# Performance work log

Measured on AMD Instinct MI355X. Metric: run time of the kernel, lower is better.

Reference implementation:

```python
import jax, jax.numpy as jnp
import numpy as np

B, N, DEG = 128, 512, 8          # graphs, nodes per graph, avg degree
E = B * N * DEG                  # 524288 edges
F_IN, H1, H2, C = 128, 64, 128, 10
RATIO = 0.8
K = int(np.ceil(RATIO * N))      # TopKPooling keeps ceil(0.8*N)=410 nodes per graph


def setup_inputs() -> dict:
    key = jax.random.key(0)
    ks = jax.random.split(key, 10)
    n_nodes = B * N
    x = jax.random.normal(ks[0], (n_nodes, F_IN), dtype=jnp.float32)
    # random intra-graph edges, then offset node ids per graph
    src = jax.random.randint(ks[1], (B, N * DEG), 0, N)
    dst = jax.random.randint(ks[2], (B, N * DEG), 0, N)
    off = (jnp.arange(B) * N)[:, None]
    edge_index = jnp.stack([(src + off).reshape(-1), (dst + off).reshape(-1)]).astype(jnp.int64)
    batch = jnp.repeat(jnp.arange(B), N).astype(jnp.int64)
    s1 = 1.0 / np.sqrt(F_IN)
    s2 = 1.0 / np.sqrt(H1)
    s3 = 1.0 / np.sqrt(H2)
    return {
        "x": x,
        "edge_index": edge_index,
        "batch": batch,
        "W1": jax.random.uniform(ks[3], (F_IN, H1), jnp.float32, -s1, s1),
        "b1": jnp.zeros((H1,), jnp.float32),
        "W2": jax.random.uniform(ks[4], (H1, H2), jnp.float32, -s2, s2),
        "b2": jnp.zeros((H2,), jnp.float32),
        "pool_w": jax.random.uniform(ks[5], (H2,), jnp.float32, -s3, s3),
        "fc_W": jax.random.uniform(ks[6], (H2, C), jnp.float32, -s3, s3),
        "fc_b": jax.random.uniform(ks[7], (C,), jnp.float32, -s3, s3),
    }


def gcn_conv(x, W, b, src, dst, num_nodes):
    # PyG GCNConv: add self-loops, symmetric normalization, scatter-add aggregation
    loop = jnp.arange(num_nodes)
    src = jnp.concatenate([src, loop])
    dst = jnp.concatenate([dst, loop])
    deg = jax.ops.segment_sum(jnp.ones_like(src, dtype=x.dtype), dst, num_segments=num_nodes)
    dis = jnp.where(deg > 0, jax.lax.rsqrt(jnp.maximum(deg, 1.0)), 0.0)
    norm = dis[src] * dis[dst]                       # [E+N]
    h = x @ W                                        # transform first (smaller of the two in conv1)
    out = jax.ops.segment_sum(norm[:, None] * h[src], dst, num_segments=num_nodes)
    return out + b


def reference(x, edge_index, batch, W1, b1, W2, b2, pool_w, fc_W, fc_b):
    num_nodes = x.shape[0]
    src, dst = edge_index[0], edge_index[1]
    x = jax.nn.relu(gcn_conv(x, W1, b1, src, dst, num_nodes))
    x = jax.nn.relu(gcn_conv(x, W2, b2, src, dst, num_nodes))
    # TopKPooling: score = (x . w)/||w||, per-graph top-k on raw score, gate by tanh(score)
    score = (x @ pool_w) / jnp.linalg.norm(pool_w)   # [B*N]
    score_b = score.reshape(B, N)
    top_vals, top_idx = jax.lax.top_k(score_b, K)    # [B, K]
    x_b = x.reshape(B, N, H2)
    x_sel = jnp.take_along_axis(x_b, top_idx[:, :, None], axis=1)   # [B, K, H2]
    x_sel = x_sel * jnp.tanh(top_vals)[:, :, None]
    # global max pool over each (pooled) graph; pooled edge_index is unused downstream
    g = jnp.max(x_sel, axis=1)                        # [B, H2]
    logits = g @ fc_W + fc_b                          # [B, C]
    return jax.nn.log_softmax(logits, axis=1)
```

## Files before the change

kernel.cpp:

```cpp
#include <hip/hip_runtime.h>
#include <hip/hip_bf16.h>


#define BB 128
#define NN 512
#define NODES (BB*NN)
#define EE (BB*NN*8)
#define EDGPG (NN*8)
#define F_IN 128
#define H1 64
#define H2 128
#define NC 10
#define KSEL 410
#define ROWCAP 48

typedef unsigned short u16;
typedef unsigned int   u32;

static __device__ __forceinline__ float lo2f(u32 u){ return __uint_as_float(u << 16); }
static __device__ __forceinline__ float hi2f(u32 u){ return __uint_as_float(u & 0xffff0000u); }
static __device__ __forceinline__ u16 f2b(float f){
    __hip_bfloat16 h = __float2bfloat16(f);
    return *reinterpret_cast<u16*>(&h);
}
static __device__ __forceinline__ u32 packbf(float a, float b){
    return (u32)f2b(a) | ((u32)f2b(b) << 16);
}
static __device__ __forceinline__ void acc8s(float* a, uint4 v, float ds){
    a[0] = fmaf(ds, lo2f(v.x), a[0]); a[1] = fmaf(ds, hi2f(v.x), a[1]);
    a[2] = fmaf(ds, lo2f(v.y), a[2]); a[3] = fmaf(ds, hi2f(v.y), a[3]);
    a[4] = fmaf(ds, lo2f(v.z), a[4]); a[5] = fmaf(ds, hi2f(v.z), a[5]);
    a[6] = fmaf(ds, lo2f(v.w), a[6]); a[7] = fmaf(ds, hi2f(v.w), a[7]);
}
static __device__ __forceinline__ void acc8(float* a, uint4 v){
    a[0] += lo2f(v.x); a[1] += hi2f(v.x);
    a[2] += lo2f(v.y); a[3] += hi2f(v.y);
    a[4] += lo2f(v.z); a[5] += hi2f(v.z);
    a[6] += lo2f(v.w); a[7] += hi2f(v.w);
}
static __device__ __forceinline__ int swz2048(int bid){
    return ((bid & 7) << 8) | (bid >> 3);
}

static __device__ __forceinline__ bool ei_is_i64(const int* __restrict__ ei){
    return ((ei[1] | ei[3] | ei[5] | ei[7]) == 0);
}
static __device__ __forceinline__ int ld_src(const int* __restrict__ ei, int e, bool w64){
    return w64 ? ei[2*e] : ei[e];
}
static __device__ __forceinline__ int ld_dst(const int* __restrict__ ei, int e, bool w64){
    return w64 ? ei[2*(EE + e)] : ei[EE + e];
}

#define G1NODES 64
#define XPAD 68
__global__ __launch_bounds__(512) void k_prep_gemm1(const int* __restrict__ ei,
                                                    const float* __restrict__ x,
                                                    const float* __restrict__ W1,
                                                    int* __restrict__ cnt,
                                                    int* __restrict__ adj,
                                                    u32* __restrict__ h1u){
    __shared__ __align__(16) float Ws[64*H1];
    __shared__ __align__(16) float xs[G1NODES*XPAD];
    bool w64 = ei_is_i64(ei);
    int t = threadIdx.x;
    int gb = (int)blockIdx.x;
    int b  = gb >> 3;
    int sub = gb & 7;
    int node0 = b*NN + sub*G1NODES;

    {
        int e = b*EDGPG + sub*512 + t;
        int d = (ld_dst(ei, e, w64) - b*NN) & (NN - 1);
        int s = ld_src(ei, e, w64) & (NODES - 1);
        int node = b*NN + d;
        int p = atomicAdd(&cnt[node], 1);
        if (p < ROWCAP - 1) adj[node*ROWCAP + 1 + p] = s;
    }
    if (t < G1NODES){
        int node = node0 + t;
        adj[node*ROWCAP] = node;
    }

    int tc = t & 15, tr = t >> 4;
    int j0 = tc*4, n0 = tr*2;
    float acc[2][4] = {};
    for (int half = 0; half < 2; ++half){
        const float4* Wv = (const float4*)(W1 + half*4096);
        for (int i = t; i < 1024; i += 512)
            *(float4*)&Ws[i*4] = Wv[i];
        for (int i = t; i < 1024; i += 512){
            int node = i >> 4, c = i & 15;
            float4 v = *(const float4*)(x + (size_t)(node0 + node)*F_IN + half*64 + c*4);
            *(float4*)&xs[node*XPAD + c*4] = v;
        }
        __syncthreads();
        #pragma unroll 2
        for (int k = 0; k < 64; k += 4){
            float4 xv0 = *(const float4*)&xs[(n0+0)*XPAD + k];
            float4 xv1 = *(const float4*)&xs[(n0+1)*XPAD + k];
            float xa0[4] = {xv0.x, xv0.y, xv0.z, xv0.w};
            float xa1[4] = {xv1.x, xv1.y, xv1.z, xv1.w};
            #pragma unroll
            for (int kk = 0; kk < 4; ++kk){
                float4 wv = *(const float4*)&Ws[(k+kk)*H1 + j0];
                acc[0][0] += xa0[kk]*wv.x; acc[0][1] += xa0[kk]*wv.y; acc[0][2] += xa0[kk]*wv.z; acc[0][3] += xa0[kk]*wv.w;
                acc[1][0] += xa1[kk]*wv.x; acc[1][1] += xa1[kk]*wv.y; acc[1][2] += xa1[kk]*wv.z; acc[1][3] += xa1[kk]*wv.w;
            }
        }
        __syncthreads();
    }
    #pragma unroll
    for (int i = 0; i < 2; ++i){
        int node = node0 + n0 + i;
        size_t base = (size_t)node*32 + tc*2;
        h1u[base]     = packbf(acc[i][0], acc[i][1]);
        h1u[base + 1] = packbf(acc[i][2], acc[i][3]);
    }
}

__global__ __launch_bounds__(256) void k_agg1(const uint4* __restrict__ h1v,
                                              const int* __restrict__ cnt,
                                              const int* __restrict__ adj,
                                              const float4* __restrict__ b1v,
                                              uint4* __restrict__ a1v){
    __shared__ float disl[NN];
    int t = threadIdx.x;
    int lb = swz2048((int)blockIdx.x);
    int node0 = lb*32;
    int gbase = node0 & ~(NN - 1);
    for (int i = t; i < NN; i += 256){
        int c = cnt[gbase + i]; if (c > ROWCAP-1) c = ROWCAP-1;
        disl[i] = rsqrtf((float)(c + 1));
    }
    __syncthreads();
    int node = node0 + (t >> 3);
    int fl = t & 7;
    int rs = node*ROWCAP;
    int c = cnt[node]; if (c > ROWCAP-1) c = ROWCAP-1;
    int pe = rs + c + 1;
    float a0[8] = {}, a1r[8] = {}, a2r[8] = {}, a3r[8] = {};
    int p = rs;
    for (; p + 4 <= pe; p += 4){
        int s0 = adj[p], s1 = adj[p+1], s2 = adj[p+2], s3 = adj[p+3];
        float d0 = disl[s0 & (NN-1)], d1 = disl[s1 & (NN-1)];
        float d2 = disl[s2 & (NN-1)], d3 = disl[s3 & (NN-1)];
        uint4 v0 = h1v[s0*8 + fl];
        uint4 v1 = h1v[s1*8 + fl];
        uint4 v2 = h1v[s2*8 + fl];
        uint4 v3 = h1v[s3*8 + fl];
        acc8s(a0, v0, d0); acc8s(a1r, v1, d1); acc8s(a2r, v2, d2); acc8s(a3r, v3, d3);
    }
    for (; p < pe; ++p){
        int s = adj[p];
        acc8s(a0, h1v[s*8 + fl], disl[s & (NN-1)]);
    }
    float r[8];
    #pragma unroll
    for (int j = 0; j < 8; ++j) r[j] = (a0[j] + a1r[j]) + (a2r[j] + a3r[j]);
    float dn = disl[node & (NN-1)];
    float4 bA = b1v[2*fl], bB = b1v[2*fl+1];
    float w0 = dn*r[0] + bA.x; w0 = w0 > 0.f ? w0 : 0.f;
    float w1 = dn*r[1] + bA.y; w1 = w1 > 0.f ? w1 : 0.f;
    float w2 = dn*r[2] + bA.z; w2 = w2 > 0.f ? w2 : 0.f;
    float w3 = dn*r[3] + bA.w; w3 = w3 > 0.f ? w3 : 0.f;
    float w4 = dn*r[4] + bB.x; w4 = w4 > 0.f ? w4 : 0.f;
    float w5 = dn*r[5] + bB.y; w5 = w5 > 0.f ? w5 : 0.f;
    float w6 = dn*r[6] + bB.z; w6 = w6 > 0.f ? w6 : 0.f;
    float w7 = dn*r[7] + bB.w; w7 = w7 > 0.f ? w7 : 0.f;
    a1v[node*8 + fl] = make_uint4(packbf(dn*w0, dn*w1), packbf(dn*w2, dn*w3),
                                  packbf(dn*w4, dn*w5), packbf(dn*w6, dn*w7));
}

#define G2NODES 32
#define APAD 68
__global__ __launch_bounds__(256) void k_gemm2s(const uint4* __restrict__ a1v,
                                                const int* __restrict__ cnt,
                                                const int* __restrict__ adj,
                                                const float* __restrict__ W2,
                                                const float* __restrict__ b2,
                                                const float* __restrict__ pw,
                                                u32* __restrict__ a2u,
                                                float* __restrict__ score){
    __shared__ __align__(16) float Ws[32*H2];
    __shared__ __align__(16) float as[G2NODES*APAD];
    __shared__ float pws[H2];
    int t = threadIdx.x;
    int lb = swz2048((int)blockIdx.x);
    int node0 = lb*G2NODES;
    if (t < H2) pws[t] = pw[t];
    {
        int fl = t & 7, nl = t >> 3;
        int node = node0 + nl;
        int rs = node*ROWCAP;
        int c = cnt[node]; if (c > ROWCAP-1) c = ROWCAP-1;
        int pe = rs + c + 1;
        float a0[8] = {}, a1r[8] = {}, a2r[8] = {}, a3r[8] = {};
        int p = rs;
        for (; p + 4 <= pe; p += 4){
            int s0 = adj[p], s1 = adj[p+1], s2 = adj[p+2], s3 = adj[p+3];
            uint4 v0 = a1v[s0*8 + fl];
            uint4 v1 = a1v[s1*8 + fl];
            uint4 v2 = a1v[s2*8 + fl];
            uint4 v3 = a1v[s3*8 + fl];
            acc8(a0, v0); acc8(a1r, v1); acc8(a2r, v2); acc8(a3r, v3);
        }
        for (; p < pe; ++p){
            uint4 v = a1v[adj[p]*8 + fl];
            acc8(a0, v);
        }
        float dn = rsqrtf((float)(c + 1));
        float* dst = &as[nl*APAD + 8*fl];
        float r0 = dn*((a0[0] + a1r[0]) + (a2r[0] + a3r[0]));
        float r1 = dn*((a0[1] + a1r[1]) + (a2r[1] + a3r[1]));
        float r2 = dn*((a0[2] + a1r[2]) + (a2r[2] + a3r[2]));
        float r3 = dn*((a0[3] + a1r[3]) + (a2r[3] + a3r[3]));
        float r4 = dn*((a0[4] + a1r[4]) + (a2r[4] + a3r[4]));
        float r5 = dn*((a0[5] + a1r[5]) + (a2r[5] + a3r[5]));
        float r6 = dn*((a0[6] + a1r[6]) + (a2r[6] + a3r[6]));
        float r7 = dn*((a0[7] + a1r[7]) + (a2r[7] + a3r[7]));
        *(float4*)&dst[0] = make_float4(r0, r1, r2, r3);
        *(float4*)&dst[4] = make_float4(r4, r5, r6, r7);
    }
    int tc = t & 31, tr = t >> 5;
    int j0 = tc*4, n0 = tr*4;
    float acc[4][4] = {};
    for (int half = 0; half < 2; ++half){
        const float4* Wv = (const float4*)(W2 + half*4096);
        for (int i = t; i < 1024; i += 256)
            *(float4*)&Ws[i*4] = Wv[i];
        __syncthreads();
        int kb = half*32;
        #pragma unroll 2
        for (int k = 0; k < 32; k += 4){
            float4 xv0 = *(const float4*)&as[(n0+0)*APAD + kb + k];
            float4 xv1 = *(const float4*)&as[(n0+1)*APAD + kb + k];
            float4 xv2 = *(const float4*)&as[(n0+2)*APAD + kb + k];
            float4 xv3 = *(const float4*)&as[(n0+3)*APAD + kb + k];
            float xa0[4] = {xv0.x, xv0.y, xv0.z, xv0.w};
            float xa1[4] = {xv1.x, xv1.y, xv1.z, xv1.w};
            float xa2[4] = {xv2.x, xv2.y, xv2.z, xv2.w};
            float xa3[4] = {xv3.x, xv3.y, xv3.z, xv3.w};
            #pragma unroll
            for (int kk = 0; kk < 4; ++kk){
                float4 wv = *(const float4*)&Ws[(k+kk)*H2 + j0];
                acc[0][0] += xa0[kk]*wv.x; acc[0][1] += xa0[kk]*wv.y; acc[0][2] += xa0[kk]*wv.z; acc[0][3] += xa0[kk]*wv.w;
                acc[1][0] += xa1[kk]*wv.x; acc[1][1] += xa1[kk]*wv.y; acc[1][2] += xa1[kk]*wv.z; acc[1][3] += xa1[kk]*wv.w;
                acc[2][0] += xa2[kk]*wv.x; acc[2][1] += xa2[kk]*wv.y; acc[2][2] += xa2[kk]*wv.z; acc[2][3] += xa2[kk]*wv.w;
                acc[3][0] += xa3[kk]*wv.x; acc[3][1] += xa3[kk]*wv.y; acc[3][2] += xa3[kk]*wv.z; acc[3][3] += xa3[kk]*wv.w;
            }
        }
        __syncthreads();
    }
    float p0 = pws[j0], p1 = pws[j0+1], p2 = pws[j0+2], p3 = pws[j0+3];
    float bj0 = b2[j0], bj1 = b2[j0+1], bj2 = b2[j0+2], bj3 = b2[j0+3];
    #pragma unroll
    for (int i = 0; i < 4; ++i){
        float v0 = acc[i][0] + bj0; v0 = v0 > 0.f ? v0 : 0.f;
        float v1 = acc[i][1] + bj1; v1 = v1 > 0.f ? v1 : 0.f;
        float v2 = acc[i][2] + bj2; v2 = v2 > 0.f ? v2 : 0.f;
        float v3 = acc[i][3] + bj3; v3 = v3 > 0.f ? v3 : 0.f;
        size_t base = (size_t)(node0 + n0 + i)*64 + tc*2;
        a2u[base]     = packbf(v0, v1);
        a2u[base + 1] = packbf(v2, v3);
        float sp = v0*p0 + v1*p1 + v2*p2 + v3*p3;
        sp += __shfl_xor(sp, 16, 32);
        sp += __shfl_xor(sp,  8, 32);
        sp += __shfl_xor(sp,  4, 32);
        sp += __shfl_xor(sp,  2, 32);
        sp += __shfl_xor(sp,  1, 32);
        if (tc == 0) score[node0 + n0 + i] = sp;
    }
}

__global__ __launch_bounds__(512) void k_pool(const u32* __restrict__ a2u,
                                              const float* __restrict__ score,
                                              const float* __restrict__ pw,
                                              const float* __restrict__ fcW,
                                              const float* __restrict__ fcb,
                                              float* __restrict__ out){
    __shared__ float so[NN];
    __shared__ float ss[NN];
    __shared__ float th[NN];
    __shared__ float pm[32*H2];
    __shared__ float gl[H2];
    __shared__ float fws[H2*NC];
    __shared__ float lg[NC];
    __shared__ float red[3];
    int b = blockIdx.x, t = threadIdx.x;
    for (int i = t; i < H2*NC; i += 512) fws[i] = fcW[i];
    if (t < H2){ float v = pw[t]; gl[t] = v*v; }
    __syncthreads();
    if (t == 0){
        float s = 0.f;
        for (int i = 0; i < H2; ++i) s += gl[i];
        red[2] = rsqrtf(s);
    }
    __syncthreads();
    float pwinv = red[2];
    float sc = score[b*NN + t];
    so[t] = sc; ss[t] = sc; th[t] = tanhf(sc*pwinv);
    __syncthreads();
    for (int k = 2; k <= NN; k <<= 1){
        for (int j = k >> 1; j > 0; j >>= 1){
            int ixj = t ^ j;
            if (ixj > t){
                float a = ss[t], c = ss[ixj];
                bool desc = ((t & k) == 0);
                bool sw = desc ? (a < c) : (a > c);
                if (sw){ ss[t] = c; ss[ixj] = a; }
            }
            __syncthreads();
        }
    }
    float thresh = ss[KSEL-1];
    float mask_t = (so[t] >= thresh) ? 0.f : -INFINITY;
    __syncthreads();
    so[t] = mask_t;
    __syncthreads();
    int tc = t & 15, q = t >> 4;
    const uint4* ap = (const uint4*)(a2u + (size_t)b*NN*64);
    float m0 = -INFINITY, m1 = -INFINITY, m2 = -INFINITY, m3 = -INFINITY;
    float m4 = -INFINITY, m5 = -INFINITY, m6 = -INFINITY, m7 = -INFINITY;
    int nb = q*16;
    #pragma unroll 4
    for (int n = nb; n < nb + 16; ++n){
        uint4 v = ap[(size_t)n*16 + tc];
        float thn = th[n], son = so[n];
        m0 = fmaxf(m0, lo2f(v.x)*thn + son);
        m1 = fmaxf(m1, hi2f(v.x)*thn + son);
        m2 = fmaxf(m2, lo2f(v.y)*thn + son);
        m3 = fmaxf(m3, hi2f(v.y)*thn + son);
        m4 = fmaxf(m4, lo2f(v.z)*thn + son);
        m5 = fmaxf(m5, hi2f(v.z)*thn + son);
        m6 = fmaxf(m6, lo2f(v.w)*thn + son);
        m7 = fmaxf(m7, hi2f(v.w)*thn + son);
    }
    float* pmr = &pm[q*H2 + 8*tc];
    pmr[0] = m0; pmr[1] = m1; pmr[2] = m2; pmr[3] = m3;
    pmr[4] = m4; pmr[5] = m5; pmr[6] = m6; pmr[7] = m7;
    __syncthreads();
    if (t < H2){
        float g = pm[t];
        #pragma unroll
        for (int qq = 1; qq < 32; ++qq) g = fmaxf(g, pm[qq*H2 + t]);
        gl[t] = g;
    }
    __syncthreads();
    if (t < NC){
        float acc = fcb[t];
        for (int k2 = 0; k2 < H2; ++k2) acc += gl[k2]*fws[k2*NC + t];
        lg[t] = acc;
    }
    __syncthreads();
    if (t == 0){
        float mx = lg[0];
        for (int i = 1; i < NC; ++i) mx = fmaxf(mx, lg[i]);
        float s = 0.f;
        for (int i = 0; i < NC; ++i) s += expf(lg[i] - mx);
        red[0] = mx; red[1] = logf(s);
    }
    __syncthreads();
    if (t < NC) out[b*NC + t] = lg[t] - red[0] - red[1];
}

extern "C" void kernel_launch(void* const* d_in, const int* in_sizes, int n_in,
                              void* d_out, int out_size, void* d_ws, size_t ws_size,
                              hipStream_t stream) {
    const float* x   = (const float*)d_in[0];
    const int*   ei  = (const int*)d_in[1];
    const float* W1  = (const float*)d_in[3];
    const float* b1  = (const float*)d_in[4];
    const float* W2  = (const float*)d_in[5];
    const float* b2  = (const float*)d_in[6];
    const float* pw  = (const float*)d_in[7];
    const float* fcW = (const float*)d_in[8];
    const float* fcb = (const float*)d_in[9];

    char* ws = (char*)d_ws;
    int*   cnt   = (int*)(ws + 4096);
    float* score = (float*)(ws + 524288);
    int*   adj   = (int*)(ws + 4194304);
    u32*   h1u   = (u32*)(ws + 16777216);
    u32*   a1u   = (u32*)(ws + 25165824);
    u32*   a2u   = (u32*)(ws + 33554432);

    hipMemsetAsync(cnt, 0, NODES*sizeof(int), stream);
    k_prep_gemm1<<<NODES/G1NODES, 512, 0, stream>>>(ei, x, W1, cnt, adj, h1u);
    k_agg1<<<NODES/32, 256, 0, stream>>>((const uint4*)h1u, cnt, adj,
                                         (const float4*)b1, (uint4*)a1u);
    k_gemm2s<<<NODES/G2NODES, 256, 0, stream>>>((const uint4*)a1u, cnt, adj,
                                                W2, b2, pw, a2u, score);
    k_pool<<<BB, 512, 0, stream>>>(a2u, score, pw, fcW, fcb, (float*)d_out);
}
```

Measured before the change: 173.8 us.

## Fuse GCN pipeline into two per-graph kernels with LDS-resident features

Replaces the four-kernel pipeline with two kernels that each run one 1024-thread block per graph. The first builds the adjacency (as u16 local ids) with LDS atomics, runs the W1 GEMM into a shared bf16 buffer, and aggregates conv1 from LDS. The second keeps a1, W2, scores and activations in LDS and fuses conv2 aggregation, the GEMM, scoring, top-k selection, gated max-pool and the FC/log-softmax. The goal is to remove the memset, the global h1, a2 and score round-trips and three kernel launch boundaries. In exchange, only 128 blocks run, which leaves many CUs idle. LDS use per block is close to the hardware limit, so each block runs long and serialized.

```diff
diff --git a/kernel.cpp b/kernel.cpp
--- a/kernel.cpp
+++ b/kernel.cpp
@@ -4,7 +4,6 @@
 
 #define BB 128
 #define NN 512
-#define NODES (BB*NN)
 #define EE (BB*NN*8)
 #define EDGPG (NN*8)
 #define F_IN 128
@@ -26,20 +25,25 @@
 static __device__ __forceinline__ u32 packbf(float a, float b){
     return (u32)f2b(a) | ((u32)f2b(b) << 16);
 }
-static __device__ __forceinline__ void acc8s(float* a, uint4 v, float ds){
-    a[0] = fmaf(ds, lo2f(v.x), a[0]); a[1] = fmaf(ds, hi2f(v.x), a[1]);
-    a[2] = fmaf(ds, lo2f(v.y), a[2]); a[3] = fmaf(ds, hi2f(v.y), a[3]);
-    a[4] = fmaf(ds, lo2f(v.z), a[4]); a[5] = fmaf(ds, hi2f(v.z), a[5]);
-    a[6] = fmaf(ds, lo2f(v.w), a[6]); a[7] = fmaf(ds, hi2f(v.w), a[7]);
-}
 static __device__ __forceinline__ void acc8(float* a, uint4 v){
     a[0] += lo2f(v.x); a[1] += hi2f(v.x);
     a[2] += lo2f(v.y); a[3] += hi2f(v.y);
     a[4] += lo2f(v.z); a[5] += hi2f(v.z);
     a[6] += lo2f(v.w); a[7] += hi2f(v.w);
 }
-static __device__ __forceinline__ int swz2048(int bid){
-    return ((bid & 7) << 8) | (bid >> 3);
+static __device__ __forceinline__ void acc32s(float* a, const u32* hrow, float ds){
+    #pragma unroll
+    for (int q = 0; q < 4; ++q){
+        uint4 v = *(const uint4*)(hrow + q*4);
+        a[q*8+0] = fmaf(ds, lo2f(v.x), a[q*8+0]);
+        a[q*8+1] = fmaf(ds, hi2f(v.x), a[q*8+1]);
+        a[q*8+2] = fmaf(ds, lo2f(v.y), a[q*8+2]);
+        a[q*8+3] = fmaf(ds, hi2f(v.y), a[q*8+3]);
+        a[q*8+4] = fmaf(ds, lo2f(v.z), a[q*8+4]);
+        a[q*8+5] = fmaf(ds, hi2f(v.z), a[q*8+5]);
+        a[q*8+6] = fmaf(ds, lo2f(v.w), a[q*8+6]);
+        a[q*8+7] = fmaf(ds, hi2f(v.w), a[q*8+7]);
+    }
 }
 
 static __device__ __forceinline__ bool ei_is_i64(const int* __restrict__ ei){
@@ -52,305 +56,315 @@
     return w64 ? ei[2*(EE + e)] : ei[EE + e];
 }
 
-#define G1NODES 64
-#define XPAD 68
-__global__ __launch_bounds__(512) void k_prep_gemm1(const int* __restrict__ ei,
-                                                    const float* __restrict__ x,
-                                                    const float* __restrict__ W1,
-                                                    int* __restrict__ cnt,
-                                                    int* __restrict__ adj,
-                                                    u32* __restrict__ h1u){
-    __shared__ __align__(16) float Ws[64*H1];
-    __shared__ __align__(16) float xs[G1NODES*XPAD];
+#define XP2 132
+#define H1R 36
+
+__global__ __launch_bounds__(1024) void k_conv1(const int* __restrict__ ei,
+                                                const float* __restrict__ x,
+                                                const float* __restrict__ W1,
+                                                const float* __restrict__ b1,
+                                                u16* __restrict__ adjG,
+                                                int* __restrict__ cntG,
+                                                uint4* __restrict__ a1u){
+    __shared__ int   cntL[NN];
+    __shared__ float disl[NN];
+    __shared__ float b1s[H1];
+    __shared__ __align__(16) float Ws[F_IN*H1];
+    __shared__ __align__(16) float xs[64*XP2];
+    __shared__ __align__(16) u32   h1g[NN*H1R];
     bool w64 = ei_is_i64(ei);
     int t = threadIdx.x;
-    int gb = (int)blockIdx.x;
-    int b  = gb >> 3;
-    int sub = gb & 7;
-    int node0 = b*NN + sub*G1NODES;
-
+    int g = blockIdx.x;
+
+    if (t < NN) cntL[t] = 0;
+    if (t < H1) b1s[t] = b1[t];
     {
-        int e = b*EDGPG + sub*512 + t;
-        int d = (ld_dst(ei, e, w64) - b*NN) & (NN - 1);
-        int s = ld_src(ei, e, w64) & (NODES - 1);
-        int node = b*NN + d;
-        int p = atomicAdd(&cnt[node], 1);
-        if (p < ROWCAP - 1) adj[node*ROWCAP + 1 + p] = s;
-    }
-    if (t < G1NODES){
-        int node = node0 + t;
-        adj[node*ROWCAP] = node;
-    }
+        const float4* Wv = (const float4*)W1;
+        *(float4*)&Ws[t*4]          = Wv[t];
+        *(float4*)&Ws[(t+1024)*4]   = Wv[t+1024];
+    }
+    __syncthreads();
+
+    #pragma unroll
+    for (int i = 0; i < 4; ++i){
+        int e = g*EDGPG + i*1024 + t;
+        int d = (ld_dst(ei, e, w64) - g*NN) & (NN - 1);
+        int s =  ld_src(ei, e, w64) & (NN - 1);
+        int p = atomicAdd(&cntL[d], 1);
+        if (p < ROWCAP - 1) adjG[(size_t)(g*NN + d)*ROWCAP + 1 + p] = (u16)s;
+    }
+    if (t < NN) adjG[(size_t)(g*NN + t)*ROWCAP] = (u16)t;
 
     int tc = t & 15, tr = t >> 4;
-    int j0 = tc*4, n0 = tr*2;
-    float acc[2][4] = {};
-    for (int half = 0; half < 2; ++half){
-        const float4* Wv = (const float4*)(W1 + half*4096);
-        for (int i = t; i < 1024; i += 512)
-            *(float4*)&Ws[i*4] = Wv[i];
-        for (int i = t; i < 1024; i += 512){
-            int node = i >> 4, c = i & 15;
-            float4 v = *(const float4*)(x + (size_t)(node0 + node)*F_IN + half*64 + c*4);
-            *(float4*)&xs[node*XPAD + c*4] = v;
+    int j0 = tc*4;
+    for (int c = 0; c < 8; ++c){
+        #pragma unroll
+        for (int kf = 0; kf < 2; ++kf){
+            int idx = t + kf*1024;
+            int row = idx >> 5, cf = idx & 31;
+            float4 v = *(const float4*)(x + (size_t)(g*NN + c*64 + row)*F_IN + cf*4);
+            *(float4*)&xs[row*XP2 + cf*4] = v;
         }
         __syncthreads();
-        #pragma unroll 2
-        for (int k = 0; k < 64; k += 4){
-            float4 xv0 = *(const float4*)&xs[(n0+0)*XPAD + k];
-            float4 xv1 = *(const float4*)&xs[(n0+1)*XPAD + k];
+        float a0 = 0.f, a1_ = 0.f, a2_ = 0.f, a3_ = 0.f;
+        #pragma unroll 4
+        for (int k = 0; k < F_IN; k += 4){
+            float4 xv = *(const float4*)&xs[tr*XP2 + k];
+            float xa[4] = {xv.x, xv.y, xv.z, xv.w};
+            #pragma unroll
+            for (int kk = 0; kk < 4; ++kk){
+                float4 wv = *(const float4*)&Ws[(k+kk)*H1 + j0];
+                a0 += xa[kk]*wv.x; a1_ += xa[kk]*wv.y;
+                a2_ += xa[kk]*wv.z; a3_ += xa[kk]*wv.w;
+            }
+        }
+        u32* hp = &h1g[(c*64 + tr)*H1R + tc*2];
+        hp[0] = packbf(a0, a1_);
+        hp[1] = packbf(a2_, a3_);
+        __syncthreads();
+    }
+
+    if (t < NN){
+        int c2 = cntL[t]; if (c2 > ROWCAP-1) c2 = ROWCAP-1;
+        cntG[g*NN + t] = c2;
+        disl[t] = rsqrtf((float)(c2 + 1));
+    }
+    __syncthreads();
+
+    {
+        int node = t >> 1, fl = t & 1;
+        int pe = cntL[node]; if (pe > ROWCAP-1) pe = ROWCAP-1;
+        pe += 1;
+        const u16* row = adjG + (size_t)(g*NN + node)*ROWCAP;
+        float acc[32] = {};
+        int p = 0;
+        for (; p + 4 <= pe; p += 4){
+            int s0 = row[p], s1 = row[p+1], s2 = row[p+2], s3 = row[p+3];
+            acc32s(acc, &h1g[s0*H1R + fl*16], disl[s0]);
+            acc32s(acc, &h1g[s1*H1R + fl*16], disl[s1]);
+            acc32s(acc, &h1g[s2*H1R + fl*16], disl[s2]);
+            acc32s(acc, &h1g[s3*H1R + fl*16], disl[s3]);
+        }
+        for (; p < pe; ++p){
+            int s = row[p];
+            acc32s(acc, &h1g[s*H1R + fl*16], disl[s]);
+        }
+        float dn = disl[node];
+        #pragma unroll
+        for (int q = 0; q < 4; ++q){
+            float v0 = fmaf(dn, acc[8*q+0], b1s[fl*32+8*q+0]); v0 = v0 > 0.f ? v0 : 0.f;
+            float v1 = fmaf(dn, acc[8*q+1], b1s[fl*32+8*q+1]); v1 = v1 > 0.f ? v1 : 0.f;
+            float v2 = fmaf(dn, acc[8*q+2], b1s[fl*32+8*q+2]); v2 = v2 > 0.f ? v2 : 0.f;
+            float v3 = fmaf(dn, acc[8*q+3], b1s[fl*32+8*q+3]); v3 = v3 > 0.f ? v3 : 0.f;
+            float v4 = fmaf(dn, acc[8*q+4], b1s[fl*32+8*q+4]); v4 = v4 > 0.f ? v4 : 0.f;
+            float v5 = fmaf(dn, acc[8*q+5], b1s[fl*32+8*q+5]); v5 = v5 > 0.f ? v5 : 0.f;
+            float v6 = fmaf(dn, acc[8*q+6], b1s[fl*32+8*q+6]); v6 = v6 > 0.f ? v6 : 0.f;
+            float v7 = fmaf(dn, acc[8*q+7], b1s[fl*32+8*q+7]); v7 = v7 > 0.f ? v7 : 0.f;
+            a1u[(size_t)(g*NN + node)*8 + fl*4 + q] =
+                make_uint4(packbf(dn*v0, dn*v1), packbf(dn*v2, dn*v3),
+                           packbf(dn*v4, dn*v5), packbf(dn*v6, dn*v7));
+        }
+    }
+}
+
+#define A1R 9
+#define AP2 68
+
+__global__ __launch_bounds__(1024) void k_conv2pool(const uint4* __restrict__ a1u,
+                                                    const u16* __restrict__ adjG,
+                                                    const int* __restrict__ cntG,
+                                                    const float* __restrict__ W2,
+                                                    const float* __restrict__ b2,
+                                                    const float* __restrict__ pw,
+                                                    const float* __restrict__ fcW,
+                                                    const float* __restrict__ fcb,
+                                                    float* __restrict__ out){
+    __shared__ __align__(16) uint4 a1g[NN*A1R];
+    __shared__ __align__(16) float W2pm[64*H2];
+    __shared__ __align__(16) float ass[128*AP2];
+    __shared__ float pws[H2], b2s[H2], gl[H2];
+    __shared__ int   cnti[NN];
+    __shared__ float disl[NN];
+    __shared__ float score_s[NN], th[NN], so[NN], ssort[NN];
+    __shared__ float fws[H2*NC];
+    __shared__ float lg[NC];
+    __shared__ float red[4];
+    int t = threadIdx.x;
+    int g = blockIdx.x;
+
+    #pragma unroll
+    for (int kf = 0; kf < 4; ++kf){
+        int idx = t + kf*1024;
+        a1g[(idx >> 3)*A1R + (idx & 7)] = a1u[(size_t)g*NN*8 + idx];
+    }
+    {
+        const float4* Wv = (const float4*)W2;
+        *(float4*)&W2pm[t*4]        = Wv[t];
+        *(float4*)&W2pm[(t+1024)*4] = Wv[t+1024];
+    }
+    if (t < H2){ pws[t] = pw[t]; b2s[t] = b2[t]; }
+    if (t < NN){
+        int c = cntG[g*NN + t];
+        cnti[t] = c;
+        disl[t] = rsqrtf((float)(c + 1));
+    }
+    for (int i = t; i < H2*NC; i += 1024) fws[i] = fcW[i];
+    __syncthreads();
+
+    int tc = t & 15, tr = t >> 4;
+    int j0 = tc*8;
+    u32 a2r[4][2][4];
+
+    #pragma unroll
+    for (int c = 0; c < 4; ++c){
+        {
+            int fl = t & 7, nl = t >> 3;
+            int node = c*128 + nl;
+            int pe = cnti[node] + 1;
+            const u16* row = adjG + (size_t)(g*NN + node)*ROWCAP;
+            float a0[8] = {}, b0[8] = {}, c0[8] = {}, d0[8] = {};
+            int p = 0;
+            for (; p + 4 <= pe; p += 4){
+                int s0 = row[p], s1 = row[p+1], s2 = row[p+2], s3 = row[p+3];
+                uint4 v0 = a1g[s0*A1R + fl];
+                uint4 v1 = a1g[s1*A1R + fl];
+                uint4 v2 = a1g[s2*A1R + fl];
+                uint4 v3 = a1g[s3*A1R + fl];
+                acc8(a0, v0); acc8(b0, v1); acc8(c0, v2); acc8(d0, v3);
+            }
+            for (; p < pe; ++p) acc8(a0, a1g[row[p]*A1R + fl]);
+            float dn = disl[node];
+            float* dst = &ass[nl*AP2 + fl*8];
+            float r0 = dn*((a0[0]+b0[0]) + (c0[0]+d0[0]));
+            float r1 = dn*((a0[1]+b0[1]) + (c0[1]+d0[1]));
+            float r2 = dn*((a0[2]+b0[2]) + (c0[2]+d0[2]));
+            float r3 = dn*((a0[3]+b0[3]) + (c0[3]+d0[3]));
+            float r4 = dn*((a0[4]+b0[4]) + (c0[4]+d0[4]));
+            float r5 = dn*((a0[5]+b0[5]) + (c0[5]+d0[5]));
+            float r6 = dn*((a0[6]+b0[6]) + (c0[6]+d0[6]));
+            float r7 = dn*((a0[7]+b0[7]) + (c0[7]+d0[7]));
+            *(float4*)&dst[0] = make_float4(r0, r1, r2, r3);
+            *(float4*)&dst[4] = make_float4(r4, r5, r6, r7);
+        }
+        __syncthreads();
+        float acc[2][8] = {};
+        #pragma unroll 4
+        for (int k = 0; k < H1; k += 4){
+            float4 xv0 = *(const float4*)&ass[(tr     )*AP2 + k];
+            float4 xv1 = *(const float4*)&ass[(tr + 64)*AP2 + k];
             float xa0[4] = {xv0.x, xv0.y, xv0.z, xv0.w};
             float xa1[4] = {xv1.x, xv1.y, xv1.z, xv1.w};
             #pragma unroll
             for (int kk = 0; kk < 4; ++kk){
-                float4 wv = *(const float4*)&Ws[(k+kk)*H1 + j0];
-                acc[0][0] += xa0[kk]*wv.x; acc[0][1] += xa0[kk]*wv.y; acc[0][2] += xa0[kk]*wv.z; acc[0][3] += xa0[kk]*wv.w;
-                acc[1][0] += xa1[kk]*wv.x; acc[1][1] += xa1[kk]*wv.y; acc[1][2] += xa1[kk]*wv.z; acc[1][3] += xa1[kk]*wv.w;
-            }
+                float4 wa = *(const float4*)&W2pm[(k+kk)*H2 + j0];
+                float4 wb = *(const float4*)&W2pm[(k+kk)*H2 + j0 + 4];
+                acc[0][0] += xa0[kk]*wa.x; acc[0][1] += xa0[kk]*wa.y;
+                acc[0][2] += xa0[kk]*wa.z; acc[0][3] += xa0[kk]*wa.w;
+                acc[0][4] += xa0[kk]*wb.x; acc[0][5] += xa0[kk]*wb.y;
+                acc[0][6] += xa0[kk]*wb.z; acc[0][7] += xa0[kk]*wb.w;
+                acc[1][0] += xa1[kk]*wa.x; acc[1][1] += xa1[kk]*wa.y;
+                acc[1][2] += xa1[kk]*wa.z; acc[1][3] += xa1[kk]*wa.w;
+                acc[1][4] += xa1[kk]*wb.x; acc[1][5] += xa1[kk]*wb.y;
+                acc[1][6] += xa1[kk]*wb.z; acc[1][7] += xa1[kk]*wb.w;
+            }
+        }
+        #pragma unroll
+        for (int r2 = 0; r2 < 2; ++r2){
+            float v0 = acc[r2][0] + b2s[j0+0]; v0 = v0 > 0.f ? v0 : 0.f;
+            float v1 = acc[r2][1] + b2s[j0+1]; v1 = v1 > 0.f ? v1 : 0.f;
+            float v2 = acc[r2][2] + b2s[j0+2]; v2 = v2 > 0.f ? v2 : 0.f;
+            float v3 = acc[r2][3] + b2s[j0+3]; v3 = v3 > 0.f ? v3 : 0.f;
+            float v4 = acc[r2][4] + b2s[j0+4]; v4 = v4 > 0.f ? v4 : 0.f;
+            float v5 = acc[r2][5] + b2s[j0+5]; v5 = v5 > 0.f ? v5 : 0.f;
+            float v6 = acc[r2][6] + b2s[j0+6]; v6 = v6 > 0.f ? v6 : 0.f;
+            float v7 = acc[r2][7] + b2s[j0+7]; v7 = v7 > 0.f ? v7 : 0.f;
+            a2r[c][r2][0] = packbf(v0, v1);
+            a2r[c][r2][1] = packbf(v2, v3);
+            a2r[c][r2][2] = packbf(v4, v5);
+            a2r[c][r2][3] = packbf(v6, v7);
+            float sp = v0*pws[j0] + v1*pws[j0+1] + v2*pws[j0+2] + v3*pws[j0+3]
+                     + v4*pws[j0+4] + v5*pws[j0+5] + v6*pws[j0+6] + v7*pws[j0+7];
+            sp += __shfl_xor(sp, 8, 16);
+            sp += __shfl_xor(sp, 4, 16);
+            sp += __shfl_xor(sp, 2, 16);
+            sp += __shfl_xor(sp, 1, 16);
+            if (tc == 0) score_s[c*128 + tr + r2*64] = sp;
         }
         __syncthreads();
     }
-    #pragma unroll
-    for (int i = 0; i < 2; ++i){
-        int node = node0 + n0 + i;
-        size_t base = (size_t)node*32 + tc*2;
-        h1u[base]     = packbf(acc[i][0], acc[i][1]);
-        h1u[base + 1] = packbf(acc[i][2], acc[i][3]);
-    }
-}
-
-__global__ __launch_bounds__(256) void k_agg1(const uint4* __restrict__ h1v,
-                                              const int* __restrict__ cnt,
-                                              const int* __restrict__ adj,
-                                              const float4* __restrict__ b1v,
-                                              uint4* __restrict__ a1v){
-    __shared__ float disl[NN];
-    int t = threadIdx.x;
-    int lb = swz2048((int)blockIdx.x);
-    int node0 = lb*32;
-    int gbase = node0 & ~(NN - 1);
-    for (int i = t; i < NN; i += 256){
-        int c = cnt[gbase + i]; if (c > ROWCAP-1) c = ROWCAP-1;
-        disl[i] = rsqrtf((float)(c + 1));
-    }
-    __syncthreads();
-    int node = node0 + (t >> 3);
-    int fl = t & 7;
-    int rs = node*ROWCAP;
-    int c = cnt[node]; if (c > ROWCAP-1) c = ROWCAP-1;
-    int pe = rs + c + 1;
-    float a0[8] = {}, a1r[8] = {}, a2r[8] = {}, a3r[8] = {};
-    int p = rs;
-    for (; p + 4 <= pe; p += 4){
-        int s0 = adj[p], s1 = adj[p+1], s2 = adj[p+2], s3 = adj[p+3];
-        float d0 = disl[s0 & (NN-1)], d1 = disl[s1 & (NN-1)];
-        float d2 = disl[s2 & (NN-1)], d3 = disl[s3 & (NN-1)];
-        uint4 v0 = h1v[s0*8 + fl];
-        uint4 v1 = h1v[s1*8 + fl];
-        uint4 v2 = h1v[s2*8 + fl];
-        uint4 v3 = h1v[s3*8 + fl];
-        acc8s(a0, v0, d0); acc8s(a1r, v1, d1); acc8s(a2r, v2, d2); acc8s(a3r, v3, d3);
-    }
-    for (; p < pe; ++p){
-        int s = adj[p];
-        acc8s(a0, h1v[s*8 + fl], disl[s & (NN-1)]);
-    }
-    float r[8];
-    #pragma unroll
-    for (int j = 0; j < 8; ++j) r[j] = (a0[j] + a1r[j]) + (a2r[j] + a3r[j]);
-    float dn = disl[node & (NN-1)];
-    float4 bA = b1v[2*fl], bB = b1v[2*fl+1];
-    float w0 = dn*r[0] + bA.x; w0 = w0 > 0.f ? w0 : 0.f;
-    float w1 = dn*r[1] + bA.y; w1 = w1 > 0.f ? w1 : 0.f;
-    float w2 = dn*r[2] + bA.z; w2 = w2 > 0.f ? w2 : 0.f;
-    float w3 = dn*r[3] + bA.w; w3 = w3 > 0.f ? w3 : 0.f;
-    float w4 = dn*r[4] + bB.x; w4 = w4 > 0.f ? w4 : 0.f;
-    float w5 = dn*r[5] + bB.y; w5 = w5 > 0.f ? w5 : 0.f;
-    float w6 = dn*r[6] + bB.z; w6 = w6 > 0.f ? w6 : 0.f;
-    float w7 = dn*r[7] + bB.w; w7 = w7 > 0.f ? w7 : 0.f;
-    a1v[node*8 + fl] = make_uint4(packbf(dn*w0, dn*w1), packbf(dn*w2, dn*w3),
-                                  packbf(dn*w4, dn*w5), packbf(dn*w6, dn*w7));
-}
-
-#define G2NODES 32
-#define APAD 68
-__global__ __launch_bounds__(256) void k_gemm2s(const uint4* __restrict__ a1v,
-                                                const int* __restrict__ cnt,
-                                                const int* __restrict__ adj,
-                                                const float* __restrict__ W2,
-                                                const float* __restrict__ b2,
-                                                const float* __restrict__ pw,
-                                                u32* __restrict__ a2u,
-                                                float* __restrict__ score){
-    __shared__ __align__(16) float Ws[32*H2];
-    __shared__ __align__(16) float as[G2NODES*APAD];
-    __shared__ float pws[H2];
-    int t = threadIdx.x;
-    int lb = swz2048((int)blockIdx.x);
-    int node0 = lb*G2NODES;
-    if (t < H2) pws[t] = pw[t];
+
+    if (t == 0){
+        float s2 = 0.f;
+        for (int i = 0; i < H2; ++i) s2 += pws[i]*pws[i];
+        red[2] = rsqrtf(s2);
+    }
+    __syncthreads();
+    float v = (t < NN) ? score_s[t] : -INFINITY;
+    for (int k2 = 2; k2 <= NN; k2 <<= 1){
+        for (int j = k2 >> 1; j > 0; j >>= 1){
+            float cc;
+            if (j >= 64){
+                if (t < NN) ssort[t] = v;
+                __syncthreads();
+                cc = (t < NN) ? ssort[t ^ j] : -INFINITY;
+                __syncthreads();
+            } else {
+                cc = __shfl_xor(v, j, 64);
+            }
+            if (t < NN){
+                bool desc  = ((t & k2) == 0);
+                bool lower = ((t & j) == 0);
+                bool wantmax = (desc == lower);
+                v = wantmax ? fmaxf(v, cc) : fminf(v, cc);
+            }
+        }
+    }
+    if (t < NN) ssort[t] = v;
+    __syncthreads();
+    float thresh = ssort[KSEL-1];
+    if (t < NN){
+        float sc = score_s[t];
+        so[t] = (sc >= thresh) ? 0.f : -INFINITY;
+        th[t] = tanhf(sc*red[2]);
+    }
+    __syncthreads();
     {
-        int fl = t & 7, nl = t >> 3;
-        int node = node0 + nl;
-        int rs = node*ROWCAP;
-        int c = cnt[node]; if (c > ROWCAP-1) c = ROWCAP-1;
-        int pe = rs + c + 1;
-        float a0[8] = {}, a1r[8] = {}, a2r[8] = {}, a3r[8] = {};
-        int p = rs;
-        for (; p + 4 <= pe; p += 4){
-            int s0 = adj[p], s1 = adj[p+1], s2 = adj[p+2], s3 = adj[p+3];
-            uint4 v0 = a1v[s0*8 + fl];
-            uint4 v1 = a1v[s1*8 + fl];
-            uint4 v2 = a1v[s2*8 + fl];
-            uint4 v3 = a1v[s3*8 + fl];
-            acc8(a0, v0); acc8(a1r, v1); acc8(a2r, v2); acc8(a3r, v3);
-        }
-        for (; p < pe; ++p){
-            uint4 v = a1v[adj[p]*8 + fl];
-            acc8(a0, v);
-        }
-        float dn = rsqrtf((float)(c + 1));
-        float* dst = &as[nl*APAD + 8*fl];
-        float r0 = dn*((a0[0] + a1r[0]) + (a2r[0] + a3r[0]));
-        float r1 = dn*((a0[1] + a1r[1]) + (a2r[1] + a3r[1]));
-        float r2 = dn*((a0[2] + a1r[2]) + (a2r[2] + a3r[2]));
-        float r3 = dn*((a0[3] + a1r[3]) + (a2r[3] + a3r[3]));
-        float r4 = dn*((a0[4] + a1r[4]) + (a2r[4] + a3r[4]));
-        float r5 = dn*((a0[5] + a1r[5]) + (a2r[5] + a3r[5]));
-        float r6 = dn*((a0[6] + a1r[6]) + (a2r[6] + a3r[6]));
-        float r7 = dn*((a0[7] + a1r[7]) + (a2r[7] + a3r[7]));
-        *(float4*)&dst[0] = make_float4(r0, r1, r2, r3);
-        *(float4*)&dst[4] = make_float4(r4, r5, r6, r7);
-    }
-    int tc = t & 31, tr = t >> 5;
-    int j0 = tc*4, n0 = tr*4;
-    float acc[4][4] = {};
-    for (int half = 0; half < 2; ++half){
-        const float4* Wv = (const float4*)(W2 + half*4096);
-        for (int i = t; i < 1024; i += 256)
-            *(float4*)&Ws[i*4] = Wv[i];
-        __syncthreads();
-        int kb = half*32;
-        #pragma unroll 2
-        for (int k = 0; k < 32; k += 4){
-            float4 xv0 = *(const float4*)&as[(n0+0)*APAD + kb + k];
-            float4 xv1 = *(const float4*)&as[(n0+1)*APAD + kb + k];
-            float4 xv2 = *(const float4*)&as[(n0+2)*APAD + kb + k];
-            float4 xv3 = *(const float4*)&as[(n0+3)*APAD + kb + k];
-            float xa0[4] = {xv0.x, xv0.y, xv0.z, xv0.w};
-            float xa1[4] = {xv1.x, xv1.y, xv1.z, xv1.w};
-            float xa2[4] = {xv2.x, xv2.y, xv2.z, xv2.w};
-            float xa3[4] = {xv3.x, xv3.y, xv3.z, xv3.w};
+        float m0 = -INFINITY, m1 = -INFINITY, m2 = -INFINITY, m3 = -INFINITY;
+        float m4 = -INFINITY, m5 = -INFINITY, m6 = -INFINITY, m7 = -INFINITY;
+        #pragma unroll
+        for (int c = 0; c < 4; ++c){
             #pragma unroll
-            for (int kk = 0; kk < 4; ++kk){
-                float4 wv = *(const float4*)&Ws[(k+kk)*H2 + j0];
-                acc[0][0] += xa0[kk]*wv.x; acc[0][1] += xa0[kk]*wv.y; acc[0][2] += xa0[kk]*wv.z; acc[0][3] += xa0[kk]*wv.w;
-                acc[1][0] += xa1[kk]*wv.x; acc[1][1] += xa1[kk]*wv.y; acc[1][2] += xa1[kk]*wv.z; acc[1][3] += xa1[kk]*wv.w;
-                acc[2][0] += xa2[kk]*wv.x; acc[2][1] += xa2[kk]*wv.y; acc[2][2] += xa2[kk]*wv.z; acc[2][3] += xa2[kk]*wv.w;
-                acc[3][0] += xa3[kk]*wv.x; acc[3][1] += xa3[kk]*wv.y; acc[3][2] += xa3[kk]*wv.z; acc[3][3] += xa3[kk]*wv.w;
-            }
-        }
-        __syncthreads();
-    }
-    float p0 = pws[j0], p1 = pws[j0+1], p2 = pws[j0+2], p3 = pws[j0+3];
-    float bj0 = b2[j0], bj1 = b2[j0+1], bj2 = b2[j0+2], bj3 = b2[j0+3];
-    #pragma unroll
-    for (int i = 0; i < 4; ++i){
-        float v0 = acc[i][0] + bj0; v0 = v0 > 0.f ? v0 : 0.f;
-        float v1 = acc[i][1] + bj1; v1 = v1 > 0.f ? v1 : 0.f;
-        float v2 = acc[i][2] + bj2; v2 = v2 > 0.f ? v2 : 0.f;
-        float v3 = acc[i][3] + bj3; v3 = v3 > 0.f ? v3 : 0.f;
-        size_t base = (size_t)(node0 + n0 + i)*64 + tc*2;
-        a2u[base]     = packbf(v0, v1);
-        a2u[base + 1] = packbf(v2, v3);
-        float sp = v0*p0 + v1*p1 + v2*p2 + v3*p3;
-        sp += __shfl_xor(sp, 16, 32);
-        sp += __shfl_xor(sp,  8, 32);
-        sp += __shfl_xor(sp,  4, 32);
-        sp += __shfl_xor(sp,  2, 32);
-        sp += __shfl_xor(sp,  1, 32);
-        if (tc == 0) score[node0 + n0 + i] = sp;
-    }
-}
-
-__global__ __launch_bounds__(512) void k_pool(const u32* __restrict__ a2u,
-                                              const float* __restrict__ score,
-                                              const float* __restrict__ pw,
-                                              const float* __restrict__ fcW,
-                                              const float* __restrict__ fcb,
-                                              float* __restrict__ out){
-    __shared__ float so[NN];
-    __shared__ float ss[NN];
-    __shared__ float th[NN];
-    __shared__ float pm[32*H2];
-    __shared__ float gl[H2];
-    __shared__ float fws[H2*NC];
-    __shared__ float lg[NC];
-    __shared__ float red[3];
-    int b = blockIdx.x, t = threadIdx.x;
-    for (int i = t; i < H2*NC; i += 512) fws[i] = fcW[i];
-    if (t < H2){ float v = pw[t]; gl[t] = v*v; }
-    __syncthreads();
-    if (t == 0){
-        float s = 0.f;
-        for (int i = 0; i < H2; ++i) s += gl[i];
-        red[2] = rsqrtf(s);
-    }
-    __syncthreads();
-    float pwinv = red[2];
-    float sc = score[b*NN + t];
-    so[t] = sc; ss[t] = sc; th[t] = tanhf(sc*pwinv);
-    __syncthreads();
-    for (int k = 2; k <= NN; k <<= 1){
-        for (int j = k >> 1; j > 0; j >>= 1){
-            int ixj = t ^ j;
-            if (ixj > t){
-                float a = ss[t], c = ss[ixj];
-                bool desc = ((t & k) == 0);
-                bool sw = desc ? (a < c) : (a > c);
-                if (sw){ ss[t] = c; ss[ixj] = a; }
-            }
-            __syncthreads();
-        }
-    }
-    float thresh = ss[KSEL-1];
-    float mask_t = (so[t] >= thresh) ? 0.f : -INFINITY;
-    __syncthreads();
-    so[t] = mask_t;
-    __syncthreads();
-    int tc = t & 15, q = t >> 4;
-    const uint4* ap = (const uint4*)(a2u + (size_t)b*NN*64);
-    float m0 = -INFINITY, m1 = -INFINITY, m2 = -INFINITY, m3 = -INFINITY;
-    float m4 = -INFINITY, m5 = -INFINITY, m6 = -INFINITY, m7 = -INFINITY;
-    int nb = q*16;
-    #pragma unroll 4
-    for (int n = nb; n < nb + 16; ++n){
-        uint4 v = ap[(size_t)n*16 + tc];
-        float thn = th[n], son = so[n];
-        m0 = fmaxf(m0, lo2f(v.x)*thn + son);
-        m1 = fmaxf(m1, hi2f(v.x)*thn + son);
-        m2 = fmaxf(m2, lo2f(v.y)*thn + son);
-        m3 = fmaxf(m3, hi2f(v.y)*thn + son);
-        m4 = fmaxf(m4, lo2f(v.z)*thn + son);
-        m5 = fmaxf(m5, hi2f(v.z)*thn + son);
-        m6 = fmaxf(m6, lo2f(v.w)*thn + son);
-        m7 = fmaxf(m7, hi2f(v.w)*thn + son);
-    }
-    float* pmr = &pm[q*H2 + 8*tc];
-    pmr[0] = m0; pmr[1] = m1; pmr[2] = m2; pmr[3] = m3;
-    pmr[4] = m4; pmr[5] = m5; pmr[6] = m6; pmr[7] = m7;
+            for (int r2 = 0; r2 < 2; ++r2){
+                int node = c*128 + tr + r2*64;
+                float thn = th[node], son = so[node];
+                u32 q0 = a2r[c][r2][0], q1 = a2r[c][r2][1];
+                u32 q2 = a2r[c][r2][2], q3 = a2r[c][r2][3];
+                m0 = fmaxf(m0, lo2f(q0)*thn + son);
+                m1 = fmaxf(m1, hi2f(q0)*thn + son);
+                m2 = fmaxf(m2, lo2f(q1)*thn + son);
+                m3 = fmaxf(m3, hi2f(q1)*thn + son);
+                m4 = fmaxf(m4, lo2f(q2)*thn + son);
+                m5 = fmaxf(m5, hi2f(q2)*thn + son);
+                m6 = fmaxf(m6, lo2f(q3)*thn + son);
+                m7 = fmaxf(m7, hi2f(q3)*thn + son);
+            }
+        }
+        float* pmr = &W2pm[tr*H2 + j0];
+        pmr[0] = m0; pmr[1] = m1; pmr[2] = m2; pmr[3] = m3;
+        pmr[4] = m4; pmr[5] = m5; pmr[6] = m6; pmr[7] = m7;
+    }
     __syncthreads();
     if (t < H2){
-        float g = pm[t];
+        float gm = W2pm[t];
         #pragma unroll
-        for (int qq = 1; qq < 32; ++qq) g = fmaxf(g, pm[qq*H2 + t]);
-        gl[t] = g;
+        for (int q = 1; q < 64; ++q) gm = fmaxf(gm, W2pm[q*H2 + t]);
+        gl[t] = gm;
     }
     __syncthreads();
     if (t < NC){
-        float acc = fcb[t];
-        for (int k2 = 0; k2 < H2; ++k2) acc += gl[k2]*fws[k2*NC + t];
-        lg[t] = acc;
+        float a = fcb[t];
+        for (int k2 = 0; k2 < H2; ++k2) a += gl[k2]*fws[k2*NC + t];
+        lg[t] = a;
     }
     __syncthreads();
     if (t == 0){
@@ -361,7 +375,7 @@
         red[0] = mx; red[1] = logf(s);
     }
     __syncthreads();
-    if (t < NC) out[b*NC + t] = lg[t] - red[0] - red[1];
+    if (t < NC) out[g*NC + t] = lg[t] - red[0] - red[1];
 }
 
 extern "C" void kernel_launch(void* const* d_in, const int* in_sizes, int n_in,
@@ -378,18 +392,11 @@
     const float* fcb = (const float*)d_in[9];
 
     char* ws = (char*)d_ws;
-    int*   cnt   = (int*)(ws + 4096);
-    float* score = (float*)(ws + 524288);
-    int*   adj   = (int*)(ws + 4194304);
-    u32*   h1u   = (u32*)(ws + 16777216);
-    u32*   a1u   = (u32*)(ws + 25165824);
-    u32*   a2u   = (u32*)(ws + 33554432);
-
-    hipMemsetAsync(cnt, 0, NODES*sizeof(int), stream);
-    k_prep_gemm1<<<NODES/G1NODES, 512, 0, stream>>>(ei, x, W1, cnt, adj, h1u);
-    k_agg1<<<NODES/32, 256, 0, stream>>>((const uint4*)h1u, cnt, adj,
-                                         (const float4*)b1, (uint4*)a1u);
-    k_gemm2s<<<NODES/G2NODES, 256, 0, stream>>>((const uint4*)a1u, cnt, adj,
-                                                W2, b2, pw, a2u, score);
-    k_pool<<<BB, 512, 0, stream>>>(a2u, score, pw, fcW, fcb, (float*)d_out);
-}
+    u16*   adjG = (u16*)(ws + 4096);
+    int*   cntG = (int*)(ws + 8388608);
+    uint4* a1u  = (uint4*)(ws + 16777216);
+
+    k_conv1<<<BB, 1024, 0, stream>>>(ei, x, W1, b1, adjG, cntG, a1u);
+    k_conv2pool<<<BB, 1024, 0, stream>>>(a1u, adjG, cntG, W2, b2, pw,
+                                         fcW, fcb, (float*)d_out);
+}
```

Measured after the change: 221.0 us. +27.1%, slower.

## Use wavefront shuffles in bitonic sort, overlap edge atomics with GEMM, swizzle pool blocks

Applied to the files above, without the earlier changes.

The bitonic sort in the pooling kernel now keeps each value in a register. It exchanges partners with wavefront shuffles when the stride is below 64 and goes through shared memory only for larger strides, which removes most block-wide barriers. In the prep kernel, the adjacency atomicAdd is moved inside the GEMM loop after the first tile load, and the adjacency store is deferred to the end, so atomic latency can overlap with compute. Pool block indices are also remapped with a swizzle to change how graphs are assigned to blocks. The risks are extra register pressure and a changed memory access order.

```diff
diff --git a/kernel.cpp b/kernel.cpp
--- a/kernel.cpp
+++ b/kernel.cpp
@@ -69,18 +69,11 @@
     int sub = gb & 7;
     int node0 = b*NN + sub*G1NODES;
 
-    {
-        int e = b*EDGPG + sub*512 + t;
-        int d = (ld_dst(ei, e, w64) - b*NN) & (NN - 1);
-        int s = ld_src(ei, e, w64) & (NODES - 1);
-        int node = b*NN + d;
-        int p = atomicAdd(&cnt[node], 1);
-        if (p < ROWCAP - 1) adj[node*ROWCAP + 1 + p] = s;
-    }
-    if (t < G1NODES){
-        int node = node0 + t;
-        adj[node*ROWCAP] = node;
-    }
+    int e = b*EDGPG + sub*512 + t;
+    int dv = (ld_dst(ei, e, w64) - b*NN) & (NN - 1);
+    int sv = ld_src(ei, e, w64) & (NODES - 1);
+    int anode = b*NN + dv;
+    int p = ROWCAP;
 
     int tc = t & 15, tr = t >> 4;
     int j0 = tc*4, n0 = tr*2;
@@ -95,6 +88,8 @@
             *(float4*)&xs[node*XPAD + c*4] = v;
         }
         __syncthreads();
+        if (half == 0)
+            p = atomicAdd(&cnt[anode], 1);
         #pragma unroll 2
         for (int k = 0; k < 64; k += 4){
             float4 xv0 = *(const float4*)&xs[(n0+0)*XPAD + k];
@@ -109,6 +104,11 @@
             }
         }
         __syncthreads();
+    }
+    if (p < ROWCAP - 1) adj[anode*ROWCAP + 1 + p] = sv;
+    if (t < G1NODES){
+        int node = node0 + t;
+        adj[node*ROWCAP] = node;
     }
     #pragma unroll
     for (int i = 0; i < 2; ++i){
@@ -287,9 +287,10 @@
     __shared__ float fws[H2*NC];
     __shared__ float lg[NC];
     __shared__ float red[3];
-    int b = blockIdx.x, t = threadIdx.x;
+    int bid = blockIdx.x, t = threadIdx.x;
+    int b = ((bid & 7) << 4) | (bid >> 3);
     for (int i = t; i < H2*NC; i += 512) fws[i] = fcW[i];
-    if (t < H2){ float v = pw[t]; gl[t] = v*v; }
+    if (t < H2){ float v2 = pw[t]; gl[t] = v2*v2; }
     __syncthreads();
     if (t == 0){
         float s = 0.f;
@@ -299,20 +300,26 @@
     __syncthreads();
     float pwinv = red[2];
     float sc = score[b*NN + t];
-    so[t] = sc; ss[t] = sc; th[t] = tanhf(sc*pwinv);
-    __syncthreads();
+    so[t] = sc; th[t] = tanhf(sc*pwinv);
+    float v = sc;
     for (int k = 2; k <= NN; k <<= 1){
         for (int j = k >> 1; j > 0; j >>= 1){
-            int ixj = t ^ j;
-            if (ixj > t){
-                float a = ss[t], c = ss[ixj];
-                bool desc = ((t & k) == 0);
-                bool sw = desc ? (a < c) : (a > c);
-                if (sw){ ss[t] = c; ss[ixj] = a; }
+            bool desc  = ((t & k) == 0);
+            bool lower = ((t & j) == 0);
+            bool wantmax = (desc == lower);
+            float c;
+            if (j >= 64){
+                ss[t] = v; __syncthreads();
+                c = ss[t ^ j];
+                __syncthreads();
+            } else {
+                c = __shfl_xor(v, j, 64);
             }
-            __syncthreads();
-        }
-    }
+            v = wantmax ? fmaxf(v, c) : fminf(v, c);
+        }
+    }
+    ss[t] = v;
+    __syncthreads();
     float thresh = ss[KSEL-1];
     float mask_t = (so[t] >= thresh) ? 0.f : -INFINITY;
     __syncthreads();
@@ -325,16 +332,16 @@
     int nb = q*16;
     #pragma unroll 4
     for (int n = nb; n < nb + 16; ++n){
-        uint4 v = ap[(size_t)n*16 + tc];
+        uint4 vv = ap[(size_t)n*16 + tc];
         float thn = th[n], son = so[n];
-        m0 = fmaxf(m0, lo2f(v.x)*thn + son);
-        m1 = fmaxf(m1, hi2f(v.x)*thn + son);
-        m2 = fmaxf(m2, lo2f(v.y)*thn + son);
-        m3 = fmaxf(m3, hi2f(v.y)*thn + son);
-        m4 = fmaxf(m4, lo2f(v.z)*thn + son);
-        m5 = fmaxf(m5, hi2f(v.z)*thn + son);
-        m6 = fmaxf(m6, lo2f(v.w)*thn + son);
-        m7 = fmaxf(m7, hi2f(v.w)*thn + son);
+        m0 = fmaxf(m0, lo2f(vv.x)*thn + son);
+        m1 = fmaxf(m1, hi2f(vv.x)*thn + son);
+        m2 = fmaxf(m2, lo2f(vv.y)*thn + son);
+        m3 = fmaxf(m3, hi2f(vv.y)*thn + son);
+        m4 = fmaxf(m4, lo2f(vv.z)*thn + son);
+        m5 = fmaxf(m5, hi2f(vv.z)*thn + son);
+        m6 = fmaxf(m6, lo2f(vv.w)*thn + son);
+        m7 = fmaxf(m7, hi2f(vv.w)*thn + son);
     }
     float* pmr = &pm[q*H2 + 8*tc];
     pmr[0] = m0; pmr[1] = m1; pmr[2] = m2; pmr[3] = m3;
```

Result: faster. 169.4 us (-2.5%).
